# Performance work log

Hardware: AMD Instinct MI355X
Metric: run time of the kernel (lower is better)

The kernel has to match this reference:

```python
import jax, jax.numpy as jnp
import numpy as np

D_MODEL = 2048
D_STATE = 64
D_CONV = 4
EXPAND = 2
HEADDIM = 64
NGROUPS = 1
CHUNK = 64
D_INNER = EXPAND * D_MODEL            # 4096
NHEADS = D_INNER // HEADDIM           # 64
D_XBC = D_INNER + 2 * NGROUPS * D_STATE
D_IN_PROJ = 2 * D_INNER + 2 * NGROUPS * D_STATE + NHEADS


def setup_inputs():
    key = jax.random.key(0)
    ks = jax.random.split(key, 8)
    B, L = 2, 4096
    u = jax.random.normal(ks[0], (B, L, D_MODEL), jnp.float32)
    W_in = jax.random.normal(ks[1], (D_IN_PROJ, D_MODEL), jnp.float32) * 0.02
    conv_w = jax.random.normal(ks[2], (D_XBC, D_CONV), jnp.float32) * 0.2
    conv_b = jnp.zeros((D_XBC,), jnp.float32)
    dt = jnp.exp(jax.random.uniform(ks[3], (NHEADS,)) * (np.log(0.1) - np.log(0.001)) + np.log(0.001))
    dt = jnp.clip(dt, 1e-4)
    dt_bias = dt + jnp.log(-jnp.expm1(-dt))
    A_log = jnp.log(jax.random.uniform(ks[4], (NHEADS,), minval=1.0, maxval=16.0))
    D_param = jnp.ones((NHEADS,), jnp.float32)
    norm_w = jnp.ones((D_INNER,), jnp.float32)
    W_out = jax.random.normal(ks[5], (D_MODEL, D_INNER), jnp.float32) * 0.02
    return dict(u=u, W_in=W_in, conv_w=conv_w, conv_b=conv_b, dt_bias=dt_bias,
                A_log=A_log, D_param=D_param, norm_w=norm_w, W_out=W_out)


def segsum(x):
    # x: (..., T) -> (..., T, T) with entry [l,s] = sum_{s< i <= l} x[i], -inf above diag
    T = x.shape[-1]
    mask_strict = jnp.tril(jnp.ones((T, T), bool), k=-1)
    mask_incl = jnp.tril(jnp.ones((T, T), bool), k=0)
    xe = jnp.where(mask_strict, x[..., :, None], 0.0)  # element [l,s] = x[l] if l>s
    xseg = jnp.cumsum(xe, axis=-2)
    return jnp.where(mask_incl, xseg, -jnp.inf)


def ssd_scan(X, A, Bm, Cm, block_len=CHUNK):
    # X: (b,L,h,p), A: (b,L,h), Bm/Cm: (b,L,h,n)
    b, seqlen, h, p = X.shape
    n = Bm.shape[-1]
    pad_len = (block_len - seqlen % block_len) % block_len
    if pad_len > 0:
        X = jnp.pad(X, ((0, 0), (0, pad_len), (0, 0), (0, 0)))
        A = jnp.pad(A, ((0, 0), (0, pad_len), (0, 0)))
        Bm = jnp.pad(Bm, ((0, 0), (0, pad_len), (0, 0), (0, 0)))
        Cm = jnp.pad(Cm, ((0, 0), (0, pad_len), (0, 0), (0, 0)))
    L = X.shape[1]
    c = L // block_len
    Xc = X.reshape(b, c, block_len, h, p)
    Ac = A.reshape(b, c, block_len, h).transpose(0, 3, 1, 2)  # (b,h,c,l)
    Bc = Bm.reshape(b, c, block_len, h, n)
    Cc = Cm.reshape(b, c, block_len, h, n)
    A_cum = jnp.cumsum(Ac, axis=-1)                           # (b,h,c,l)
    Lmat = jnp.exp(segsum(Ac))                                # (b,h,c,l,s)
    CB = jnp.einsum('bclhn,bcshn->bhcls', Cc, Bc)
    Y_diag = jnp.einsum('bhcls,bcshp->bhclp', CB * Lmat, Xc)
    decay_states = jnp.exp(A_cum[..., -1:] - A_cum)           # (b,h,c,l)
    states = jnp.einsum('bhcl,bclhn,bclhp->bhcpn', decay_states, Bc, Xc)
    init = jnp.zeros((b, h, 1, p, n), X.dtype)
    states = jnp.concatenate([init, states], axis=2)          # (b,h,c+1,p,n)
    chunk_decay = jnp.pad(A_cum[..., -1], ((0, 0), (0, 0), (1, 0)))  # (b,h,c+1)
    decay_chunk = jnp.exp(segsum(chunk_decay))                # (b,h,c+1,c+1)
    new_states = jnp.einsum('bhzc,bhcpn->bhzpn', decay_chunk, states)[:, :, :-1]
    Y_off = jnp.einsum('bclhn,bhcpn,bhcl->bhclp', Cc, new_states, jnp.exp(A_cum))
    Y = (Y_diag + Y_off).transpose(0, 2, 3, 1, 4).reshape(b, L, h, p)
    if pad_len > 0:
        Y = Y[:, :seqlen]
    return Y


def rmsnorm_grouped(x, w, ngroups, eps=1e-5):
    gs = x.shape[-1] // ngroups
    xg = x.reshape(*x.shape[:-1], ngroups, gs)
    xg = xg * jax.lax.rsqrt(jnp.mean(xg * xg, axis=-1, keepdims=True) + eps)
    return xg.reshape(x.shape) * w


def reference(u, W_in, conv_w, conv_b, dt_bias, A_log, D_param, norm_w, W_out):
    B, L, _ = u.shape
    zxbcdt = u @ W_in.T                                      # (B,L,d_in_proj)
    z = zxbcdt[..., :D_INNER]
    xBC = zxbcdt[..., D_INNER:D_INNER + D_XBC]
    dt = zxbcdt[..., D_INNER + D_XBC:]
    # causal depthwise conv1d, kernel D_CONV, left-pad D_CONV-1
    xpad = jnp.pad(xBC, ((0, 0), (D_CONV - 1, 0), (0, 0)))
    conv = conv_b
    for k in range(D_CONV):
        conv = conv + conv_w[:, k] * xpad[:, k:k + L, :]
    xBC = jax.nn.silu(conv)
    x = xBC[..., :D_INNER].reshape(B, L, NHEADS, HEADDIM)
    B_ssm = xBC[..., D_INNER:D_INNER + NGROUPS * D_STATE].reshape(B, L, NGROUPS, D_STATE)
    C_ssm = xBC[..., D_INNER + NGROUPS * D_STATE:].reshape(B, L, NGROUPS, D_STATE)
    if NGROUPS < NHEADS:
        rep = NHEADS // NGROUPS
        B_ssm = jnp.repeat(B_ssm, rep, axis=2)
        C_ssm = jnp.repeat(C_ssm, rep, axis=2)
    dt = jax.nn.softplus(dt + dt_bias)                        # (B,L,nheads)
    A = -jnp.exp(A_log)                                       # (nheads,)
    y = ssd_scan(x * dt[..., None], A * dt, B_ssm, C_ssm, block_len=CHUNK)
    y = y + D_param[:, None] * x
    y = y.reshape(B, L, D_INNER)
    y = rmsnorm_grouped(y * jax.nn.silu(z), norm_w, NGROUPS)
    return y @ W_out.T
```

## Files before the change

### kernel.cpp

```cpp
#include <hip/hip_runtime.h>
#include <hip/hip_bf16.h>
#include <math.h>

#define SEQ       4096
#define DMODEL    2048
#define DINNER    4096
#define DXBC      4224
#define NPROJ     8384
#define NHEADS    64
#define HDIM      64
#define DSTATE    64
#define NCHUNK    64
#define XLD       4352

typedef __attribute__((ext_vector_type(8))) _Float16 half8;
typedef __attribute__((ext_vector_type(2))) _Float16 half2v;
typedef __attribute__((ext_vector_type(4))) float floatx4;

__device__ __forceinline__ void async_copy16(void* lds, const void* g) {
  __builtin_amdgcn_global_load_lds(
      (const __attribute__((address_space(1))) unsigned int*)g,
      (__attribute__((address_space(3))) unsigned int*)lds, 16, 0, 0);
}

__device__ __forceinline__ float silu_f(float x) { return x / (1.f + __expf(-x)); }

__device__ __forceinline__ void cvt8(const float* __restrict__ s, _Float16* __restrict__ d) {
  float4 a = *(const float4*)s;
  float4 b = *(const float4*)(s + 4);
  half8 h;
  h[0] = (_Float16)a.x; h[1] = (_Float16)a.y; h[2] = (_Float16)a.z; h[3] = (_Float16)a.w;
  h[4] = (_Float16)b.x; h[5] = (_Float16)b.y; h[6] = (_Float16)b.z; h[7] = (_Float16)b.w;
  *(half8*)d = h;
}

__global__ void diag_kernel(float* out, float v) { out[0] = v; }

__global__ void cvt8_kernel(const float* __restrict__ src, _Float16* __restrict__ dst, int n8) {
  int i = blockIdx.x * 256 + threadIdx.x;
  if (i < n8) cvt8(src + (size_t)i * 8, dst + (size_t)i * 8);
}

__global__ void cvt_win_kernel(const float* __restrict__ W_in, _Float16* __restrict__ dst) {
  int i = blockIdx.x * 256 + threadIdx.x;
  int row = i >> 8;
  size_t off = (size_t)i * 8;
  if (row < NPROJ) {
    cvt8(W_in + off, dst + off);
  } else {
    half8 zz = {};
    *(half8*)(dst + off) = zz;
  }
}

#define U_N8 (SEQ * DMODEL / 8)
__global__ void cvt_in_kernel(const float* __restrict__ u, const float* __restrict__ W_in,
                              _Float16* __restrict__ ubf, _Float16* __restrict__ winbf) {
  int i = blockIdx.x * 256 + threadIdx.x;
  if (i < U_N8) {
    cvt8(u + (size_t)i * 8, ubf + (size_t)i * 8);
  } else {
    int j = i - U_N8;
    int row = j >> 8;
    size_t off = (size_t)j * 8;
    if (row < NPROJ) {
      cvt8(W_in + off, winbf + off);
    } else {
      half8 zz = {};
      *(half8*)(winbf + off) = zz;
    }
  }
}

template <typename OT>
__global__ __launch_bounds__(256) void gemm_bt64(
    const _Float16* __restrict__ A, const _Float16* __restrict__ B,
    OT* __restrict__ C0, OT* __restrict__ C1, int K,
    int ldc0, int ldc1, int ncol0, int tiles_m, int tiles_n) {
  __shared__ __align__(16) _Float16 As[128 * 64];
  __shared__ __align__(16) _Float16 Bs[128 * 64];
  int t = threadIdx.x;
  int nt = tiles_m * tiles_n;
  int id = blockIdx.x;
  int id2 = ((nt & 7) == 0) ? ((id & 7) * (nt >> 3) + (id >> 3)) : id;
  int wband = tiles_m << 2;
  int g = id2 / wband;
  int rm = id2 - g * wband;
  int bw = tiles_n - (g << 2); if (bw > 4) bw = 4;
  int pn = (g << 2) + rm % bw;
  int pm = rm / bw;
  int m0 = pm * 128, n0 = pn * 128;

  int w = t >> 6, lane = t & 63, q = lane >> 4, r = lane & 15;
  int wm = (w >> 1) * 64, wn = (w & 1) * 64;
  int rowoff = lane >> 3;
  int chunkoff = ((lane & 7) ^ rowoff) * 8;
  const _Float16* gA[4];
  const _Float16* gB[4];
#pragma unroll
  for (int i = 0; i < 4; ++i) {
    gA[i] = A + (size_t)(m0 + i * 32 + w * 8 + rowoff) * K + chunkoff;
    gB[i] = B + (size_t)(n0 + i * 32 + w * 8 + rowoff) * K + chunkoff;
  }
  floatx4 acc[4][4] = {};
  for (int k0 = 0; k0 < K; k0 += 64) {
#pragma unroll
    for (int i = 0; i < 4; ++i) {
      async_copy16(As + (i * 32 + w * 8) * 64, gA[i] + k0);
      async_copy16(Bs + (i * 32 + w * 8) * 64, gB[i] + k0);
    }
    __syncthreads();
#pragma unroll
    for (int kk = 0; kk < 64; kk += 32) {
      half8 af[4], bf[4];
#pragma unroll
      for (int im = 0; im < 4; ++im) {
        int R = wm + im * 16 + r;
        af[im] = *(const half8*)&As[R * 64 + ((((kk >> 3) + q) ^ (R & 7)) << 3)];
      }
#pragma unroll
      for (int in = 0; in < 4; ++in) {
        int R = wn + in * 16 + r;
        bf[in] = *(const half8*)&Bs[R * 64 + ((((kk >> 3) + q) ^ (R & 7)) << 3)];
      }
#pragma unroll
      for (int im = 0; im < 4; ++im)
#pragma unroll
        for (int in = 0; in < 4; ++in)
          acc[im][in] =
              __builtin_amdgcn_mfma_f32_16x16x32_f16(af[im], bf[in], acc[im][in], 0, 0, 0);
    }
    __syncthreads();
  }
  OT* Cp = (n0 < ncol0) ? C0 : C1;
  int ldc = (n0 < ncol0) ? ldc0 : ldc1;
  int cb = (n0 < ncol0) ? n0 : n0 - ncol0;
#pragma unroll
  for (int im = 0; im < 4; ++im)
#pragma unroll
    for (int in = 0; in < 4; ++in)
#pragma unroll
      for (int i = 0; i < 4; ++i)
        Cp[(size_t)(m0 + wm + im * 16 + q * 4 + i) * ldc + cb + wn + in * 16 + r] =
            (OT)acc[im][in][i];
}

#define CONVB (SEQ * (DXBC / 2) / 256)
__global__ __launch_bounds__(256) void conv_dtscan_kernel(
    const _Float16* __restrict__ xin, const float* __restrict__ conv_w,
    const float* __restrict__ conv_b, _Float16* __restrict__ xcv,
    const float* __restrict__ dt_bias, const float* __restrict__ A_log,
    float* __restrict__ dtp, float* __restrict__ acum, float* __restrict__ chs) {
  int t = threadIdx.x;
  if (blockIdx.x < CONVB) {
    int idx = blockIdx.x * 256 + t;
    int l = idx / (DXBC / 2);
    int c = (idx - l * (DXBC / 2)) * 2;
    const _Float16* zc = xin + (size_t)l * XLD + c;
    float a0 = conv_b[c], a1 = conv_b[c + 1];
#pragma unroll
    for (int k = 0; k < 4; ++k) {
      int off = k - 3;
      if (l + off >= 0) {
        half2v v = *(const half2v*)(zc + (long)off * XLD);
        a0 += conv_w[c * 4 + k] * (float)v[0];
        a1 += conv_w[c * 4 + 4 + k] * (float)v[1];
      }
    }
    half2v o;
    o[0] = (_Float16)silu_f(a0);
    o[1] = (_Float16)silu_f(a1);
    *(half2v*)(xcv + (size_t)l * DXBC + c) = o;
  } else {
    __shared__ float dAs[64 * 65];
    int c = blockIdx.x - CONVB;
    int h = t & 63;
    const _Float16* dtraw = xin + DXBC;
    float bias = dt_bias[h];
    float negA = -__expf(A_log[h]);
#pragma unroll
    for (int i = 0; i < 16; ++i) {
      int l = i * 4 + (t >> 6);
      int row = c * 64 + l;
      float x = (float)dtraw[(size_t)row * XLD + h] + bias;
      float dtv = (x > 20.f) ? x : log1pf(__expf(x));
      dtp[(size_t)row * 64 + h] = dtv;
      dAs[l * 65 + h] = negA * dtv;
    }
    __syncthreads();
    if (t < 64) {
      float a = 0.f;
      size_t base = ((size_t)c * 64 + t) * 64;
      for (int l = 0; l < 64; ++l) {
        a += dAs[l * 65 + t];
        acum[base + l] = a;
      }
      chs[c * 64 + t] = a;
    }
  }
}

__global__ __launch_bounds__(256) void states_kernel(
    const _Float16* __restrict__ xcv, const float* __restrict__ dtp,
    const float* __restrict__ acum, const float* __restrict__ chs,
    _Float16* __restrict__ states) {
  int bid = blockIdx.x;
  int c = bid & 63, h = bid >> 6;
  int row0 = c * 64;
  int acbase = (c * 64 + h) * 64;
  __shared__ __align__(16) _Float16 XdT[64 * 72];
  __shared__ __align__(16) _Float16 BdT[64 * 72];
  __shared__ float dec[64];
  int t = threadIdx.x;
  if (t < 64) dec[t] = __expf(chs[acbase >> 6] - acum[acbase + t]);
  __syncthreads();
#pragma unroll
  for (int i = 0; i < 16; ++i) {
    int flat = i * 256 + t;
    int l = flat >> 6, col = flat & 63;
    int grow = row0 + l;
    float dtv = dtp[(size_t)grow * 64 + h];
    float xv = (float)xcv[(size_t)grow * DXBC + h * 64 + col] * dtv;
    XdT[col * 72 + l] = (_Float16)xv;
    float bv = (float)xcv[(size_t)grow * DXBC + DINNER + col] * dec[l];
    BdT[col * 72 + l] = (_Float16)bv;
  }
  __syncthreads();
  int w = t >> 6, lane = t & 63, q = lane >> 4, r = lane & 15;
#pragma unroll
  for (int in = 0; in < 4; ++in) {
    floatx4 a4 = {0.f, 0.f, 0.f, 0.f};
#pragma unroll
    for (int k0 = 0; k0 < 64; k0 += 32) {
      half8 af = *(const half8*)&XdT[(w * 16 + r) * 72 + k0 + q * 8];
      half8 bf = *(const half8*)&BdT[(in * 16 + r) * 72 + k0 + q * 8];
      a4 = __builtin_amdgcn_mfma_f32_16x16x32_f16(af, bf, a4, 0, 0, 0);
    }
#pragma unroll
    for (int i = 0; i < 4; ++i)
      states[((size_t)bid * 64 + (w * 16 + q * 4 + i)) * 64 + in * 16 + r] = (_Float16)a4[i];
  }
}

__global__ __launch_bounds__(256) void scan_kernel(_Float16* __restrict__ states,
                                                   const float* __restrict__ chs) {
  int bid = blockIdx.x;
  int h = bid >> 4, seg = bid & 15;
  size_t base = ((size_t)h * 64) * 4096 + seg * 256 + threadIdx.x;
  float carry = 0.f;
  float s_cur = (float)states[base];
  for (int c = 0; c < 64; ++c) {
    size_t idx = base + (size_t)c * 4096;
    float s_next = (c < 63) ? (float)states[idx + 4096] : 0.f;
    float ec = __expf(chs[c * 64 + h]);
    states[idx] = (_Float16)carry;
    carry = carry * ec + s_cur;
    s_cur = s_next;
  }
}

__global__ __launch_bounds__(256) void yout_kernel(
    const _Float16* __restrict__ xcv, const float* __restrict__ dtp,
    const float* __restrict__ acum, const _Float16* __restrict__ sin_,
    const float* __restrict__ Dp, _Float16* __restrict__ Y) {
  int bid = blockIdx.x;
  int c = bid & 63, h = bid >> 6;
  int row0 = c * 64;
  int acbase = (c * 64 + h) * 64;
  __shared__ __align__(16) _Float16 Cs[64 * 72];
  __shared__ __align__(16) _Float16 Bt[64 * 72];
  __shared__ __align__(16) _Float16 XdT[64 * 72];
  __shared__ __align__(16) _Float16 Ms[64 * 72];
  __shared__ float acs[64];
  int t = threadIdx.x;
  if (t < 64) acs[t] = acum[acbase + t];
#pragma unroll
  for (int i = 0; i < 16; ++i) {
    int flat = i * 256 + t;
    int l = flat >> 6, col = flat & 63;
    int grow = row0 + l;
    const _Float16* rp = xcv + (size_t)grow * DXBC;
    Cs[l * 72 + col] = rp[DINNER + DSTATE + col];
    Bt[l * 72 + col] = rp[DINNER + col];
    float xv = (float)rp[h * 64 + col] * dtp[(size_t)grow * 64 + h];
    XdT[col * 72 + l] = (_Float16)xv;
  }
  __syncthreads();
  int w = t >> 6, lane = t & 63, q = lane >> 4, r = lane & 15;
  int m = w * 16 + r;
#pragma unroll
  for (int in = 0; in < 4; ++in) {
    floatx4 cb = {0.f, 0.f, 0.f, 0.f};
#pragma unroll
    for (int k0 = 0; k0 < 64; k0 += 32) {
      half8 af = *(const half8*)&Cs[m * 72 + k0 + q * 8];
      half8 bf = *(const half8*)&Bt[(in * 16 + r) * 72 + k0 + q * 8];
      cb = __builtin_amdgcn_mfma_f32_16x16x32_f16(af, bf, cb, 0, 0, 0);
    }
#pragma unroll
    for (int i = 0; i < 4; ++i) {
      int l = w * 16 + q * 4 + i;
      int s = in * 16 + r;
      float v = (s <= l) ? cb[i] * __expf(acs[l] - acs[s]) : 0.f;
      Ms[l * 72 + s] = (_Float16)v;
    }
  }
  __syncthreads();
  size_t sbase = (size_t)bid * 4096;
  float Dh = Dp[h];
#pragma unroll
  for (int in = 0; in < 4; ++in) {
    floatx4 acc = {0.f, 0.f, 0.f, 0.f};
#pragma unroll
    for (int k0 = 0; k0 < 64; k0 += 32) {
      half8 af = *(const half8*)&Cs[m * 72 + k0 + q * 8];
      half8 bf = *(const half8*)&sin_[sbase + (size_t)(in * 16 + r) * 64 + k0 + q * 8];
      acc = __builtin_amdgcn_mfma_f32_16x16x32_f16(af, bf, acc, 0, 0, 0);
    }
#pragma unroll
    for (int i = 0; i < 4; ++i) acc[i] *= __expf(acs[w * 16 + q * 4 + i]);
#pragma unroll
    for (int k0 = 0; k0 < 64; k0 += 32) {
      half8 af = *(const half8*)&Ms[m * 72 + k0 + q * 8];
      half8 bf = *(const half8*)&XdT[(in * 16 + r) * 72 + k0 + q * 8];
      acc = __builtin_amdgcn_mfma_f32_16x16x32_f16(af, bf, acc, 0, 0, 0);
    }
#pragma unroll
    for (int i = 0; i < 4; ++i) {
      int l = w * 16 + q * 4 + i;
      int p = in * 16 + r;
      int grow = row0 + l;
      float xv = (float)xcv[(size_t)grow * DXBC + h * 64 + p];
      Y[(size_t)grow * DINNER + h * 64 + p] = (_Float16)(acc[i] + Dh * xv);
    }
  }
}

__global__ __launch_bounds__(256) void rmsnorm_kernel(const _Float16* __restrict__ Y,
                                                      _Float16* __restrict__ Z,
                                                      const float* __restrict__ norm_w) {
  int row = blockIdx.x;
  const half8* y8 = (const half8*)(Y + (size_t)row * DINNER);
  half8* z8 = (half8*)(Z + (size_t)row * DINNER);
  __shared__ float red[4];
  int t = threadIdx.x;
  float g[16];
  float ss = 0.f;
#pragma unroll
  for (int i = 0; i < 2; ++i) {
    int j = i * 256 + t;
    half8 yv = y8[j];
    half8 zv = z8[j];
#pragma unroll
    for (int e = 0; e < 8; ++e) {
      float gv = (float)yv[e] * silu_f((float)zv[e]);
      g[i * 8 + e] = gv;
      ss += gv * gv;
    }
  }
#pragma unroll
  for (int o = 32; o > 0; o >>= 1) ss += __shfl_down(ss, o, 64);
  if ((t & 63) == 0) red[t >> 6] = ss;
  __syncthreads();
  float rs = rsqrtf((red[0] + red[1] + red[2] + red[3]) / (float)DINNER + 1e-5f);
#pragma unroll
  for (int i = 0; i < 2; ++i) {
    int j = i * 256 + t;
    const float4* w4 = (const float4*)(norm_w + j * 8);
    float4 wa = w4[0], wb = w4[1];
    half8 o;
    o[0] = (_Float16)(g[i * 8 + 0] * rs * wa.x);
    o[1] = (_Float16)(g[i * 8 + 1] * rs * wa.y);
    o[2] = (_Float16)(g[i * 8 + 2] * rs * wa.z);
    o[3] = (_Float16)(g[i * 8 + 3] * rs * wa.w);
    o[4] = (_Float16)(g[i * 8 + 4] * rs * wb.x);
    o[5] = (_Float16)(g[i * 8 + 5] * rs * wb.y);
    o[6] = (_Float16)(g[i * 8 + 6] * rs * wb.z);
    o[7] = (_Float16)(g[i * 8 + 7] * rs * wb.w);
    z8[j] = o;
  }
}

extern "C" void kernel_launch(void* const* d_in, const int* in_sizes, int n_in,
                              void* d_out, int out_size, void* d_ws, size_t ws_size,
                              hipStream_t stream) {
  const float* u       = (const float*)d_in[0];
  const float* W_in    = (const float*)d_in[1];
  const float* conv_w  = (const float*)d_in[2];
  const float* conv_b  = (const float*)d_in[3];
  const float* dt_bias = (const float*)d_in[4];
  const float* A_log   = (const float*)d_in[5];
  const float* D_param = (const float*)d_in[6];
  const float* norm_w  = (const float*)d_in[7];
  const float* W_out   = (const float*)d_in[8];
  float* out = (float*)d_out;
  char* ws = (char*)d_ws;

  const size_t NEED_MID   = 192954368ULL;
  const size_t NEED_SMALL = 140525568ULL;
  bool big = (ws_size >= NEED_MID);
  if (!big && ws_size < NEED_SMALL) {
    diag_kernel<<<1, 1, 0, stream>>>(out, (float)ws_size);
    return;
  }

  _Float16 *winbf, *woutbf, *zb, *xbcdtb, *Yb, *xcv, *states, *ubf;
  float *dtp, *acum, *chs;
  if (big) {
    winbf  = (_Float16*)(ws + 0);
    woutbf = (_Float16*)(ws + 34603008ULL);
    zb     = (_Float16*)(ws + 51380224ULL);
    xbcdtb = (_Float16*)(ws + 84934656ULL);
    Yb     = xbcdtb;
    xcv    = (_Float16*)(ws + 120586240ULL);
    states = (_Float16*)(ws + 155189248ULL);
    ubf    = states;
    dtp    = (float*)(ws + 188743680ULL);
    acum   = (float*)(ws + 190840832ULL);
    chs    = (float*)(ws + 192937984ULL);
  } else {
    zb     = (_Float16*)(ws + 0);
    xbcdtb = (_Float16*)(ws + 33554432ULL);
    Yb     = xbcdtb;
    xcv    = (_Float16*)(ws + 69206016ULL);
    winbf  = xcv;
    states = (_Float16*)(ws + 103809024ULL);
    ubf    = states;
    woutbf = states;
    dtp    = (float*)(ws + 137363456ULL);
    acum   = (float*)(ws + 139460608ULL);
    chs    = (float*)(ws + 140509184ULL);
  }

  if (big) {
    cvt_win_kernel<<<8448, 256, 0, stream>>>(W_in, winbf);
    cvt8_kernel<<<DMODEL * DINNER / 8 / 256, 256, 0, stream>>>(
        W_out, woutbf, DMODEL * DINNER / 8);
  }

  for (int b = 0; b < 2; ++b) {
    const float* ub = u + (size_t)b * SEQ * DMODEL;
    float* outb = out + (size_t)b * SEQ * DMODEL;

    if (big) {
      cvt8_kernel<<<U_N8 / 256, 256, 0, stream>>>(ub, ubf, U_N8);
    } else {
      cvt_in_kernel<<<U_N8 / 256 + 8448, 256, 0, stream>>>(ub, W_in, ubf, winbf);
    }

    gemm_bt64<_Float16><<<32 * 66, 256, 0, stream>>>(
        ubf, winbf, zb, xbcdtb, DMODEL, DINNER, XLD, DINNER, 32, 66);

    conv_dtscan_kernel<<<CONVB + NCHUNK, 256, 0, stream>>>(
        xbcdtb, conv_w, conv_b, xcv, dt_bias, A_log, dtp, acum, chs);

    states_kernel<<<NHEADS * NCHUNK, 256, 0, stream>>>(xcv, dtp, acum, chs, states);
    scan_kernel<<<NHEADS * 16, 256, 0, stream>>>(states, chs);
    yout_kernel<<<NHEADS * NCHUNK, 256, 0, stream>>>(xcv, dtp, acum, states, D_param, Yb);

    rmsnorm_kernel<<<SEQ, 256, 0, stream>>>(Yb, zb, norm_w);

    if (!big) {
      cvt8_kernel<<<DMODEL * DINNER / 8 / 256, 256, 0, stream>>>(
          W_out, woutbf, DMODEL * DINNER / 8);
    }
    gemm_bt64<float><<<32 * 16, 256, 0, stream>>>(
        zb, woutbf, outb, outb, DINNER, DMODEL, DMODEL, 1 << 30, 32, 16);
  }
}
```

Baseline: 1.130 ms.

## Add 256x256 double-buffered GEMM and batch out-projection across both sequences

Adds a new 512-thread GEMM kernel with 256x256 tiles, XOR-swizzled LDS, double-buffered async global-to-LDS loads, grouped tile rasterization and MFMA priority hints. It is used for the z part of the input projection and for a single out-projection covering both batches, with z kept for both batches in a larger workspace. The xBC/dt columns still use the old 128-tile kernel, and W_in is now reconverted inside the per-batch conversion kernel. Larger tiles are meant to improve data reuse and cut launch and tail overhead, at the cost of fewer workgroups (256) and higher register and LDS pressure.

Measured after the change: 1.122 ms. Within noise of the previous version (-0.7%).

```diff
diff --git a/kernel.cpp b/kernel.cpp
--- a/kernel.cpp
+++ b/kernel.cpp
@@ -39,18 +39,6 @@
 __global__ void cvt8_kernel(const float* __restrict__ src, _Float16* __restrict__ dst, int n8) {
   int i = blockIdx.x * 256 + threadIdx.x;
   if (i < n8) cvt8(src + (size_t)i * 8, dst + (size_t)i * 8);
-}
-
-__global__ void cvt_win_kernel(const float* __restrict__ W_in, _Float16* __restrict__ dst) {
-  int i = blockIdx.x * 256 + threadIdx.x;
-  int row = i >> 8;
-  size_t off = (size_t)i * 8;
-  if (row < NPROJ) {
-    cvt8(W_in + off, dst + off);
-  } else {
-    half8 zz = {};
-    *(half8*)(dst + off) = zz;
-  }
 }
 
 #define U_N8 (SEQ * DMODEL / 8)
@@ -145,6 +133,105 @@
             (OT)acc[im][in][i];
 }
 
+template <typename OT>
+__global__ __launch_bounds__(512, 2) void gemm256(
+    const _Float16* __restrict__ A, const _Float16* __restrict__ B,
+    OT* __restrict__ C, int K, int ldc, int tiles_m, int tiles_n) {
+  __shared__ __align__(16) _Float16 As[2][256 * 64];
+  __shared__ __align__(16) _Float16 Bs[2][256 * 64];
+  int t = threadIdx.x;
+  int nwg = tiles_m * tiles_n;
+  int id = blockIdx.x;
+  int wgid = ((nwg & 7) == 0) ? ((id & 7) * (nwg >> 3) + (id >> 3)) : id;
+  int wband = tiles_m << 2;
+  int g = wgid / wband;
+  int rm = wgid - g * wband;
+  int bw = tiles_n - (g << 2); if (bw > 4) bw = 4;
+  int pn = (g << 2) + rm % bw;
+  int pm = rm / bw;
+  int m0 = pm * 256, n0 = pn * 256;
+
+  int w = t >> 6, lane = t & 63, q4 = lane >> 4, r16 = lane & 15;
+  int wm = (w >> 2) * 128, wn = (w & 3) * 64;
+  int srow = lane >> 3;
+  int schunk = ((lane & 7) ^ srow) << 3;
+  const _Float16* gA0 = A + (size_t)(m0 + w * 8 + srow) * K + schunk;
+  const _Float16* gB0 = B + (size_t)(n0 + w * 8 + srow) * K + schunk;
+
+  floatx4 acc[8][4] = {};
+
+  auto STAGE = [&](int buf, int kt) {
+    int k0 = kt << 6;
+#pragma unroll
+    for (int i = 0; i < 4; ++i) {
+      async_copy16(&As[buf][(i * 64 + w * 8) * 64], gA0 + (size_t)(i * 64) * K + k0);
+      async_copy16(&Bs[buf][(i * 64 + w * 8) * 64], gB0 + (size_t)(i * 64) * K + k0);
+    }
+  };
+
+  int NT = K >> 6;
+  STAGE(0, 0);
+  STAGE(1, 1);
+  asm volatile("s_waitcnt vmcnt(8)" ::: "memory");
+  __builtin_amdgcn_s_barrier();
+  asm volatile("" ::: "memory");
+
+  for (int kt = 0; kt < NT; ++kt) {
+    int cur = kt & 1;
+    const _Float16* Ab = As[cur];
+    const _Float16* Bb = Bs[cur];
+#define RD(buf_, R_, kk_) \
+  (*(const half8*)&buf_[(R_) * 64 + (((((kk_) >> 3) + q4) ^ ((R_) & 7)) << 3)])
+#define PHASE(qm, qn)                                                          \
+    {                                                                          \
+      half8 af[4][2], bf[2][2];                                                \
+      _Pragma("unroll") for (int m = 0; m < 4; ++m) {                          \
+        int R = wm + ((qm) * 4 + m) * 16 + r16;                                \
+        af[m][0] = RD(Ab, R, 0);                                               \
+        af[m][1] = RD(Ab, R, 32);                                              \
+      }                                                                        \
+      _Pragma("unroll") for (int n = 0; n < 2; ++n) {                          \
+        int R = wn + ((qn) * 2 + n) * 16 + r16;                                \
+        bf[n][0] = RD(Bb, R, 0);                                               \
+        bf[n][1] = RD(Bb, R, 32);                                              \
+      }                                                                        \
+      __builtin_amdgcn_s_setprio(1);                                           \
+      _Pragma("unroll") for (int m = 0; m < 4; ++m)                            \
+        _Pragma("unroll") for (int n = 0; n < 2; ++n) {                        \
+          acc[(qm) * 4 + m][(qn) * 2 + n] = __builtin_amdgcn_mfma_f32_16x16x32_f16( \
+              af[m][0], bf[n][0], acc[(qm) * 4 + m][(qn) * 2 + n], 0, 0, 0);   \
+          acc[(qm) * 4 + m][(qn) * 2 + n] = __builtin_amdgcn_mfma_f32_16x16x32_f16( \
+              af[m][1], bf[n][1], acc[(qm) * 4 + m][(qn) * 2 + n], 0, 0, 0);   \
+        }                                                                      \
+      __builtin_amdgcn_s_setprio(0);                                           \
+    }
+    PHASE(0, 0) PHASE(1, 0) PHASE(1, 1) PHASE(0, 1)
+#undef PHASE
+#undef RD
+    if (kt + 1 < NT) {
+      asm volatile("s_waitcnt lgkmcnt(0)" ::: "memory");
+      __builtin_amdgcn_s_barrier();
+      asm volatile("" ::: "memory");
+      if (kt + 2 < NT) {
+        STAGE(cur, kt + 2);
+        asm volatile("s_waitcnt vmcnt(8)" ::: "memory");
+      } else {
+        asm volatile("s_waitcnt vmcnt(0)" ::: "memory");
+      }
+      __builtin_amdgcn_s_barrier();
+      asm volatile("" ::: "memory");
+    }
+  }
+#pragma unroll
+  for (int m = 0; m < 8; ++m)
+#pragma unroll
+    for (int n = 0; n < 4; ++n)
+#pragma unroll
+      for (int i = 0; i < 4; ++i)
+        C[(size_t)(m0 + wm + m * 16 + q4 * 4 + i) * ldc + n0 + wn + n * 16 + r16] =
+            (OT)acc[m][n][i];
+}
+
 #define CONVB (SEQ * (DXBC / 2) / 256)
 __global__ __launch_bounds__(256) void conv_dtscan_kernel(
     const _Float16* __restrict__ xin, const float* __restrict__ conv_w,
@@ -404,67 +491,74 @@
     return;
   }
 
-  _Float16 *winbf, *woutbf, *zb, *xbcdtb, *Yb, *xcv, *states, *ubf;
-  float *dtp, *acum, *chs;
   if (big) {
-    winbf  = (_Float16*)(ws + 0);
-    woutbf = (_Float16*)(ws + 34603008ULL);
-    zb     = (_Float16*)(ws + 51380224ULL);
-    xbcdtb = (_Float16*)(ws + 84934656ULL);
-    Yb     = xbcdtb;
-    xcv    = (_Float16*)(ws + 120586240ULL);
-    states = (_Float16*)(ws + 155189248ULL);
-    ubf    = states;
-    dtp    = (float*)(ws + 188743680ULL);
-    acum   = (float*)(ws + 190840832ULL);
-    chs    = (float*)(ws + 192937984ULL);
-  } else {
-    zb     = (_Float16*)(ws + 0);
-    xbcdtb = (_Float16*)(ws + 33554432ULL);
-    Yb     = xbcdtb;
-    xcv    = (_Float16*)(ws + 69206016ULL);
-    winbf  = xcv;
-    states = (_Float16*)(ws + 103809024ULL);
-    ubf    = states;
-    woutbf = states;
-    dtp    = (float*)(ws + 137363456ULL);
-    acum   = (float*)(ws + 139460608ULL);
-    chs    = (float*)(ws + 140509184ULL);
-  }
-
-  if (big) {
-    cvt_win_kernel<<<8448, 256, 0, stream>>>(W_in, winbf);
+    _Float16* zb     = (_Float16*)(ws + 0);
+    _Float16* xbcdtb = (_Float16*)(ws + 67108864ULL);
+    _Float16* xcv    = (_Float16*)(ws + 102760448ULL);
+    _Float16* winbf  = xcv;
+    _Float16* states = (_Float16*)(ws + 137363456ULL);
+    _Float16* ubf    = states;
+    _Float16* woutbf = (_Float16*)(ws + 170917888ULL);
+    float* dtp  = (float*)(ws + 187695104ULL);
+    float* acum = (float*)(ws + 188743680ULL);
+    float* chs  = (float*)(ws + 189792256ULL);
+
     cvt8_kernel<<<DMODEL * DINNER / 8 / 256, 256, 0, stream>>>(
         W_out, woutbf, DMODEL * DINNER / 8);
-  }
-
-  for (int b = 0; b < 2; ++b) {
-    const float* ub = u + (size_t)b * SEQ * DMODEL;
-    float* outb = out + (size_t)b * SEQ * DMODEL;
-
-    if (big) {
-      cvt8_kernel<<<U_N8 / 256, 256, 0, stream>>>(ub, ubf, U_N8);
-    } else {
+
+    for (int b = 0; b < 2; ++b) {
+      const float* ub = u + (size_t)b * SEQ * DMODEL;
+      _Float16* zbb = zb + (size_t)b * SEQ * DINNER;
+
       cvt_in_kernel<<<U_N8 / 256 + 8448, 256, 0, stream>>>(ub, W_in, ubf, winbf);
-    }
-
-    gemm_bt64<_Float16><<<32 * 66, 256, 0, stream>>>(
-        ubf, winbf, zb, xbcdtb, DMODEL, DINNER, XLD, DINNER, 32, 66);
-
-    conv_dtscan_kernel<<<CONVB + NCHUNK, 256, 0, stream>>>(
-        xbcdtb, conv_w, conv_b, xcv, dt_bias, A_log, dtp, acum, chs);
-
-    states_kernel<<<NHEADS * NCHUNK, 256, 0, stream>>>(xcv, dtp, acum, chs, states);
-    scan_kernel<<<NHEADS * 16, 256, 0, stream>>>(states, chs);
-    yout_kernel<<<NHEADS * NCHUNK, 256, 0, stream>>>(xcv, dtp, acum, states, D_param, Yb);
-
-    rmsnorm_kernel<<<SEQ, 256, 0, stream>>>(Yb, zb, norm_w);
-
-    if (!big) {
+
+      gemm256<_Float16><<<256, 512, 0, stream>>>(ubf, winbf, zbb, DMODEL, DINNER, 16, 16);
+      gemm_bt64<_Float16><<<32 * 34, 256, 0, stream>>>(
+          ubf, winbf + (size_t)DINNER * DMODEL, xbcdtb, xbcdtb,
+          DMODEL, XLD, XLD, 1 << 30, 32, 34);
+
+      conv_dtscan_kernel<<<CONVB + NCHUNK, 256, 0, stream>>>(
+          xbcdtb, conv_w, conv_b, xcv, dt_bias, A_log, dtp, acum, chs);
+
+      states_kernel<<<NHEADS * NCHUNK, 256, 0, stream>>>(xcv, dtp, acum, chs, states);
+      scan_kernel<<<NHEADS * 16, 256, 0, stream>>>(states, chs);
+      yout_kernel<<<NHEADS * NCHUNK, 256, 0, stream>>>(xcv, dtp, acum, states, D_param,
+                                                       xbcdtb );
+
+      rmsnorm_kernel<<<SEQ, 256, 0, stream>>>(xbcdtb, zbb, norm_w);
+    }
+
+    gemm256<float><<<256, 512, 0, stream>>>(zb, woutbf, out, DINNER, DMODEL, 32, 8);
+  } else {
+    _Float16* zb     = (_Float16*)(ws + 0);
+    _Float16* xbcdtb = (_Float16*)(ws + 33554432ULL);
+    _Float16* Yb     = xbcdtb;
+    _Float16* xcv    = (_Float16*)(ws + 69206016ULL);
+    _Float16* winbf  = xcv;
+    _Float16* states = (_Float16*)(ws + 103809024ULL);
+    _Float16* ubf    = states;
+    _Float16* woutbf = states;
+    float* dtp  = (float*)(ws + 137363456ULL);
+    float* acum = (float*)(ws + 139460608ULL);
+    float* chs  = (float*)(ws + 140509184ULL);
+
+    for (int b = 0; b < 2; ++b) {
+      const float* ub = u + (size_t)b * SEQ * DMODEL;
+      float* outb = out + (size_t)b * SEQ * DMODEL;
+
+      cvt_in_kernel<<<U_N8 / 256 + 8448, 256, 0, stream>>>(ub, W_in, ubf, winbf);
+      gemm_bt64<_Float16><<<32 * 66, 256, 0, stream>>>(
+          ubf, winbf, zb, xbcdtb, DMODEL, DINNER, XLD, DINNER, 32, 66);
+      conv_dtscan_kernel<<<CONVB + NCHUNK, 256, 0, stream>>>(
+          xbcdtb, conv_w, conv_b, xcv, dt_bias, A_log, dtp, acum, chs);
+      states_kernel<<<NHEADS * NCHUNK, 256, 0, stream>>>(xcv, dtp, acum, chs, states);
+      scan_kernel<<<NHEADS * 16, 256, 0, stream>>>(states, chs);
+      yout_kernel<<<NHEADS * NCHUNK, 256, 0, stream>>>(xcv, dtp, acum, states, D_param, Yb);
+      rmsnorm_kernel<<<SEQ, 256, 0, stream>>>(Yb, zb, norm_w);
       cvt8_kernel<<<DMODEL * DINNER / 8 / 256, 256, 0, stream>>>(
           W_out, woutbf, DMODEL * DINNER / 8);
-    }
-    gemm_bt64<float><<<32 * 16, 256, 0, stream>>>(
-        zb, woutbf, outb, outb, DINNER, DMODEL, DMODEL, 1 << 30, 32, 16);
-  }
-}
+      gemm_bt64<float><<<32 * 16, 256, 0, stream>>>(
+          zb, woutbf, outb, outb, DINNER, DMODEL, DMODEL, 1 << 30, 32, 16);
+    }
+  }
+}
```
